# Optimization experiments

Hardware: AMD Instinct MI355X
Metric: run time of the kernel (lower is better)

## Reference

```python
import jax, jax.numpy as jnp
import numpy as np

T, B, HIMG = 16, 1024, 32
VALUE_DIM, KEY_DIM, HIDDEN, OUT_DIM = 64, 64, 512, 4


def _conv(x, w):
    # torch Conv2d(kernel=4, stride=2, padding=0)
    return jax.lax.conv_general_dilated(
        x, w, (2, 2), 'VALID', dimension_numbers=('NCHW', 'OIHW', 'NCHW'))


def setup_inputs() -> dict:
    key = jax.random.key(0)
    ks = jax.random.split(key, 24)

    def w(k, shape, s=0.05):
        return jax.random.normal(k, shape, jnp.float32) * s

    return {
        'images': jax.random.normal(ks[0], (T, B, 3, HIMG, HIMG), jnp.float32),
        # encoder
        'W1': w(ks[1], (32, 3, 4, 4)), 'b1': w(ks[2], (32,)),
        'W2': w(ks[3], (64, 32, 4, 4)), 'b2': w(ks[4], (64,)),
        'W3': w(ks[5], (64, 64, 4, 4)), 'b3': w(ks[6], (64,)),
        'We': w(ks[7], (VALUE_DIM, 4 * 64)), 'be': w(ks[8], (VALUE_DIM,)),
        # LSTMCell(key_dim+1 -> hidden), torch layout (4H, in) / (4H, H)
        'Wih': w(ks[9], (4 * HIDDEN, KEY_DIM + 1)),
        'Whh': w(ks[10], (4 * HIDDEN, HIDDEN)),
        'bih': w(ks[11], (4 * HIDDEN,)), 'bhh': w(ks[12], (4 * HIDDEN,)),
        # heads
        'Wg': w(ks[13], (1, HIDDEN)), 'bg': w(ks[14], (1,)),
        'Wk': w(ks[15], (KEY_DIM, HIDDEN)), 'bk': w(ks[16], (KEY_DIM,)),
        'Wo': w(ks[17], (OUT_DIM, HIDDEN)), 'bo': w(ks[18], (OUT_DIM,)),
        'Wc': w(ks[19], (1, 1)), 'bc': w(ks[20], (1,)),
    }


def _forward(images, W1, b1, W2, b2, W3, b3, We, be,
             Wih, Whh, bih, bhh, Wg, bg, Wk, bk, Wo, bo, Wc, bc):
    t, b = images.shape[0], images.shape[1]

    # Encoder over all frames at once (vectorized over T*B).
    # FAITHFULNESS NOTE: in the source module, the retrieved key `kr` is computed
    # but never assigned back to `kx` (kx stays k0 = zeros after step 0), so the
    # encoder output z / memory banks Mk, Mv / gate / key / confidence heads never
    # influence the returned output. We compute z here to mirror the source; it is
    # dead w.r.t. the output (XLA will DCE it under jit), exactly matching torch.
    x = images.reshape((t * b,) + images.shape[2:])
    h = jax.nn.relu(_conv(x, W1) + b1[None, :, None, None])
    h = jax.nn.relu(_conv(h, W2) + b2[None, :, None, None])
    h = jax.nn.relu(_conv(h, W3) + b3[None, :, None, None])
    z = h.reshape(t * b, -1) @ We.T + be  # (t*b, value_dim) -- dead path
    del z

    hidden = Whh.shape[1]
    kx = jnp.zeros((b, Wih.shape[1]), images.dtype)  # k0; constant every step (source bug)
    const_gates = kx @ Wih.T + bih + bhh             # (b, 4*hidden), hoisted out of the loop

    def step(carry, _):
        hx, cx = carry
        gates = const_gates + hx @ Whh.T
        i, f, g, o = jnp.split(gates, 4, axis=-1)  # torch LSTMCell gate order i,f,g,o
        cx = jax.nn.sigmoid(f) * cx + jax.nn.sigmoid(i) * jnp.tanh(g)
        hx = jax.nn.sigmoid(o) * jnp.tanh(cx)
        return (hx, cx), hx

    init = (jnp.zeros((b, hidden), images.dtype),
            jnp.zeros((b, hidden), images.dtype))
    _, hs = jax.lax.scan(step, init, None, length=t)  # (t, b, hidden)
    return hs @ Wo.T + bo  # (t, b, output_dim) == torch.stack(out)


def reference(images, W1, b1, W2, b2, W3, b3, We, be,
              Wih, Whh, bih, bhh, Wg, bg, Wk, bk, Wo, bo, Wc, bc):
    return _forward(images, W1, b1, W2, b2, W3, b3, We, be,
                    Wih, Whh, bih, bhh, Wg, bg, Wk, bk, Wo, bo, Wc, bc)
```

## Files before the change

kernel.cpp:

```cpp
#include <hip/hip_runtime.h>


#define NTHR   512
#define HID    512
#define TSTEPS 16
#define KPB    16
#define OUTB   16
#define NWORK  32

typedef unsigned long long ull;

__device__ __forceinline__ float sigm(float x) { return 1.0f / (1.0f + expf(-x)); }

__device__ __forceinline__ ull ld_xcd(const ull* p) {
  ull v;
  asm volatile("global_load_dwordx2 %0, %1, off sc0\n\ts_waitcnt vmcnt(0)"
               : "=v"(v) : "v"(p) : "memory");
  return v;
}
__device__ __forceinline__ void st_xcd(ull* p, ull v) {
  asm volatile("global_store_dwordx2 %0, %1, off sc0" :: "v"(p), "v"(v) : "memory");
}

__device__ __forceinline__ float poll_h(const ull* sL2, const ull* sLLC,
                                        int idx, unsigned tag, bool fast) {
  ull v;
  if (fast) {
    for (;;) {
      v = ld_xcd(sL2 + idx);
      if ((unsigned)(v >> 32) == tag) break;
      v = __hip_atomic_load(sLLC + idx, __ATOMIC_RELAXED,
                            __HIP_MEMORY_SCOPE_AGENT);
      if ((unsigned)(v >> 32) == tag) break;
    }
  } else {
    do {
      v = __hip_atomic_load(sLLC + idx, __ATOMIC_RELAXED,
                            __HIP_MEMORY_SCOPE_AGENT);
    } while ((unsigned)(v >> 32) != tag);
  }
  return __uint_as_float((unsigned)v);
}

__device__ __forceinline__ void publish(ull* sL2, ull* sLLC, int idx, ull pk,
                                        bool fast) {
  if (fast) st_xcd(sL2 + idx, pk);
  __hip_atomic_store(sLLC + idx, pk, __ATOMIC_RELAXED, __HIP_MEMORY_SCOPE_AGENT);
}

__global__ __launch_bounds__(NTHR, 2) void lstm_seq_kernel(
    const float* __restrict__ Whh,
    const float* __restrict__ bih,
    const float* __restrict__ bhh,
    const float* __restrict__ Wo,
    const float* __restrict__ bo,
    float* __restrict__ out,
    ull* sLLC,
    ull* sL2,
    int mode)
{
  int r;
  if (mode) {
    if (blockIdx.x & 7) return;
    r = (int)(blockIdx.x >> 3);
  } else {
    r = (int)blockIdx.x;
  }
  if (r >= NWORK) return;
  const bool fast = (mode != 0);

  const int tid = threadIdx.x;
  const int w  = tid >> 6;
  const int l  = tid & 63;
  const int g  = l >> 4;
  const int kk = l & 15;
  const int grow = g * HID + r * KPB + kk;

  __shared__ __align__(16) float chbuf[8][64];
  __shared__ float gpT[2][8][64];
  __shared__ float hstash[HID];
  __shared__ float vals[4];

  float c_state = 0.0f;
  float bs_i = 0.f, bs_f = 0.f, bs_g = 0.f, bs_o = 0.f;
  if (tid < KPB) {
    const int k = r * KPB + tid;
    bs_i = bih[k]           + bhh[k];
    bs_f = bih[HID + k]     + bhh[HID + k];
    bs_g = bih[2*HID + k]   + bhh[2*HID + k];
    bs_o = bih[3*HID + k]   + bhh[3*HID + k];
    c_state = sigm(bs_f) * 0.0f + sigm(bs_i) * tanhf(bs_g);
    const float h1 = sigm(bs_o) * tanhf(c_state);
    const ull pk = (1ull << 32) | (ull)__float_as_uint(h1);
    publish(sL2, sLLC, HID + r * KPB + tid, pk, fast);
  }

  float4 wreg[16];
  {
    const float4* Wr = reinterpret_cast<const float4*>(
        Whh + (size_t)grow * HID + w * 64);
#pragma unroll
    for (int j = 0; j < 16; ++j) wreg[j] = Wr[j];
  }

  for (int s = 2; s <= TSTEPS; ++s) {
    const int p = s & 1;

    const float h = poll_h(sL2, sLLC, (p ^ 1) * HID + w * 64 + l,
                           (unsigned)(s - 1), fast);
    if (r < OUTB - 1 && s == r + 2) hstash[w * 64 + l] = h;
    chbuf[w][l] = h;

    float4 a = make_float4(0.f, 0.f, 0.f, 0.f);
    {
      const float4* hq = reinterpret_cast<const float4*>(&chbuf[w][0]);
#pragma unroll
      for (int j = 0; j < 16; ++j) {
        const float4 h4 = hq[j];
        a.x = fmaf(wreg[j].x, h4.x, a.x);
        a.y = fmaf(wreg[j].y, h4.y, a.y);
        a.z = fmaf(wreg[j].z, h4.z, a.z);
        a.w = fmaf(wreg[j].w, h4.w, a.w);
      }
    }
    gpT[p][w][l] = (a.x + a.y) + (a.z + a.w);
    __syncthreads();

    if (tid < KPB) {
      float p0 = 0.f, p1 = 0.f, p2 = 0.f, p3 = 0.f;
#pragma unroll
      for (int j = 0; j < 8; ++j) {
        p0 += gpT[p][j][tid];
        p1 += gpT[p][j][16 + tid];
        p2 += gpT[p][j][32 + tid];
        p3 += gpT[p][j][48 + tid];
      }
      const float gi = p0 + bs_i, gf = p1 + bs_f;
      const float gg = p2 + bs_g, go = p3 + bs_o;
      c_state = sigm(gf) * c_state + sigm(gi) * tanhf(gg);
      const float hv = sigm(go) * tanhf(c_state);
      const ull pk = ((ull)(unsigned)s << 32) | (ull)__float_as_uint(hv);
      publish(sL2, sLLC, p * HID + r * KPB + tid, pk, fast);
    }
  }

  if (r >= OUTB) return;

  if (r == OUTB - 1) {
    hstash[w * 64 + l] = poll_h(sL2, sLLC, w * 64 + l, (unsigned)TSTEPS, fast);
  }
  __syncthreads();

  if (tid < 256) {
    const int wo = tid >> 6;
    const int ll = tid & 63;
    float sacc = 0.0f;
#pragma unroll
    for (int j = 0; j < 8; ++j) {
      const int k2 = ll + 64 * j;
      sacc = fmaf(Wo[wo * HID + k2], hstash[k2], sacc);
    }
#pragma unroll
    for (int m = 32; m > 0; m >>= 1) sacc += __shfl_xor(sacc, m);
    if (ll == 0) vals[wo] = sacc + bo[wo];
  }
  __syncthreads();

  const float4 vv = make_float4(vals[0], vals[1], vals[2], vals[3]);
  float4* out4 = reinterpret_cast<float4*>(out) + (size_t)r * 1024;
  out4[tid]       = vv;
  out4[tid + 512] = vv;
}

extern "C" void kernel_launch(void* const* d_in, const int* in_sizes, int n_in,
                              void* d_out, int out_size, void* d_ws, size_t ws_size,
                              hipStream_t stream) {
  const float* Whh = (const float*)d_in[10];
  const float* bih = (const float*)d_in[11];
  const float* bhh = (const float*)d_in[12];
  const float* Wo  = (const float*)d_in[17];
  const float* bo  = (const float*)d_in[18];
  float* out = (float*)d_out;

  ull* sLLC; ull* sL2; int mode; int grid;
  if (d_ws != nullptr && ws_size >= 4 * HID * sizeof(ull)) {
    sLLC = (ull*)d_ws;
    sL2  = sLLC + 2 * HID;
    mode = 1;
    grid = NWORK * 8;
  } else {
    sLLC = (ull*)(out + (size_t)out_size) - 2 * HID;
    sL2  = sLLC;
    mode = 0;
    grid = NWORK;
  }

  lstm_seq_kernel<<<dim3(grid), dim3(NTHR), 0, stream>>>(
      Whh, bih, bhh, Wo, bo, out, sLLC, sL2, mode);
}
```

Baseline: 32.97 us.

## Compute step-1 hidden state locally and overlap dual-cache poll probes

Each block now computes the full step-1 hidden vector from the biases, so the first cross-block publish and poll round trip is gone. The poll is moved to the end of each iteration. The L2 and LLC probes are issued together in one asm block so their latencies overlap instead of running in series. In exchange every thread does redundant transcendental bias work at startup, the Whh register load moves earlier, and there is a possible race where chbuf is overwritten before all warps have read it.

```diff
diff --git a/kernel.cpp b/kernel.cpp
--- a/kernel.cpp
+++ b/kernel.cpp
@@ -12,26 +12,26 @@
 
 __device__ __forceinline__ float sigm(float x) { return 1.0f / (1.0f + expf(-x)); }
 
-__device__ __forceinline__ ull ld_xcd(const ull* p) {
-  ull v;
-  asm volatile("global_load_dwordx2 %0, %1, off sc0\n\ts_waitcnt vmcnt(0)"
-               : "=v"(v) : "v"(p) : "memory");
-  return v;
-}
-__device__ __forceinline__ void st_xcd(ull* p, ull v) {
-  asm volatile("global_store_dwordx2 %0, %1, off sc0" :: "v"(p), "v"(v) : "memory");
+__device__ __forceinline__ void dual_probe(const ull* pL2, const ull* pLLC,
+                                           ull& v2, ull& vL) {
+  asm volatile(
+      "global_load_dwordx2 %0, %2, off sc0\n\t"
+      "global_load_dwordx2 %1, %3, off sc1\n\t"
+      "s_waitcnt vmcnt(0)"
+      : "=&v"(v2), "=&v"(vL)
+      : "v"(pL2), "v"(pLLC)
+      : "memory");
 }
 
 __device__ __forceinline__ float poll_h(const ull* sL2, const ull* sLLC,
                                         int idx, unsigned tag, bool fast) {
   ull v;
   if (fast) {
+    ull v2, vL;
     for (;;) {
-      v = ld_xcd(sL2 + idx);
-      if ((unsigned)(v >> 32) == tag) break;
-      v = __hip_atomic_load(sLLC + idx, __ATOMIC_RELAXED,
-                            __HIP_MEMORY_SCOPE_AGENT);
-      if ((unsigned)(v >> 32) == tag) break;
+      dual_probe(sL2 + idx, sLLC + idx, v2, vL);
+      if ((unsigned)(v2 >> 32) == tag) { v = v2; break; }
+      if ((unsigned)(vL >> 32) == tag) { v = vL; break; }
     }
   } else {
     do {
@@ -44,7 +44,10 @@
 
 __device__ __forceinline__ void publish(ull* sL2, ull* sLLC, int idx, ull pk,
                                         bool fast) {
-  if (fast) st_xcd(sL2 + idx, pk);
+  if (fast) {
+    asm volatile("global_store_dwordx2 %0, %1, off sc0"
+                 :: "v"(sL2 + idx), "v"(pk) : "memory");
+  }
   __hip_atomic_store(sLLC + idx, pk, __ATOMIC_RELAXED, __HIP_MEMORY_SCOPE_AGENT);
 }
 
@@ -81,6 +84,25 @@
   __shared__ float hstash[HID];
   __shared__ float vals[4];
 
+  float4 wreg[16];
+  {
+    const float4* Wr = reinterpret_cast<const float4*>(
+        Whh + (size_t)grow * HID + w * 64);
+#pragma unroll
+    for (int j = 0; j < 16; ++j) wreg[j] = Wr[j];
+  }
+
+  {
+    const float gi = bih[tid]           + bhh[tid];
+    const float gf = bih[HID + tid]     + bhh[HID + tid];
+    const float gg = bih[2*HID + tid]   + bhh[2*HID + tid];
+    const float go = bih[3*HID + tid]   + bhh[3*HID + tid];
+    const float c1 = sigm(gf) * 0.0f + sigm(gi) * tanhf(gg);
+    const float h1 = sigm(go) * tanhf(c1);
+    chbuf[w][l] = h1;
+    if (r == 0) hstash[tid] = h1;
+  }
+
   float c_state = 0.0f;
   float bs_i = 0.f, bs_f = 0.f, bs_g = 0.f, bs_o = 0.f;
   if (tid < KPB) {
@@ -90,26 +112,10 @@
     bs_g = bih[2*HID + k]   + bhh[2*HID + k];
     bs_o = bih[3*HID + k]   + bhh[3*HID + k];
     c_state = sigm(bs_f) * 0.0f + sigm(bs_i) * tanhf(bs_g);
-    const float h1 = sigm(bs_o) * tanhf(c_state);
-    const ull pk = (1ull << 32) | (ull)__float_as_uint(h1);
-    publish(sL2, sLLC, HID + r * KPB + tid, pk, fast);
-  }
-
-  float4 wreg[16];
-  {
-    const float4* Wr = reinterpret_cast<const float4*>(
-        Whh + (size_t)grow * HID + w * 64);
-#pragma unroll
-    for (int j = 0; j < 16; ++j) wreg[j] = Wr[j];
   }
 
   for (int s = 2; s <= TSTEPS; ++s) {
     const int p = s & 1;
-
-    const float h = poll_h(sL2, sLLC, (p ^ 1) * HID + w * 64 + l,
-                           (unsigned)(s - 1), fast);
-    if (r < OUTB - 1 && s == r + 2) hstash[w * 64 + l] = h;
-    chbuf[w][l] = h;
 
     float4 a = make_float4(0.f, 0.f, 0.f, 0.f);
     {
@@ -142,6 +148,12 @@
       const ull pk = ((ull)(unsigned)s << 32) | (ull)__float_as_uint(hv);
       publish(sL2, sLLC, p * HID + r * KPB + tid, pk, fast);
     }
+
+    if (s < TSTEPS) {
+      const float h = poll_h(sL2, sLLC, p * HID + w * 64 + l, (unsigned)s, fast);
+      if (r >= 1 && r < OUTB - 1 && s == r + 1) hstash[w * 64 + l] = h;
+      chbuf[w][l] = h;
+    }
   }
 
   if (r >= OUTB) return;
```

New measurement: 34.96 us. 1.06x slower.
